# Optimization experiments

Hardware: AMD Instinct MI355X
Metric: run time of the kernel (lower is better)

The kernel has to match this reference:

```python
import jax, jax.numpy as jnp
import numpy as np

IN_DIM, OUT_DIM, NUM, K = 128, 128, 5, 3
SIZE = IN_DIM * OUT_DIM  # number of spline activations
BATCH = 1024


def extend_grid(grid, k):
    # pykan: pad grid by k uniform steps on each side -> (size, num+1+2k)
    h = (grid[:, -1:] - grid[:, :1]) / (grid.shape[1] - 1)
    for _ in range(k):
        grid = jnp.concatenate([grid[:, :1] - h, grid, grid[:, -1:] + h], axis=1)
    return grid


def b_batch(x, grid, k):
    # Cox-de-Boor recursion, unrolled over fixed order k.
    # x: (size, batch), grid: (size, P) already extended. Returns (size, P-1-k, batch).
    x = x[:, None, :]        # (size, 1, batch)
    g = grid[:, :, None]     # (size, P, 1)
    B = ((x >= g[:, :-1]) & (x < g[:, 1:])).astype(x.dtype)  # order 0
    for p in range(1, k + 1):
        B = (x - g[:, :-(p + 1)]) / (g[:, p:-1] - g[:, :-(p + 1)]) * B[:, :-1] \
          + (g[:, p + 1:] - x) / (g[:, p + 1:] - g[:, 1:-p]) * B[:, 1:]
    return B


def setup_inputs() -> dict:
    key = jax.random.key(0)
    k1, k2 = jax.random.split(key)
    x = jax.random.normal(k1, (BATCH, IN_DIM), dtype=jnp.float32)
    # grid: identical uniform rows, as in torch.einsum('i,j->ij', ones(size), linspace)
    grid = jnp.tile(jnp.linspace(-1.0, 1.0, NUM + 1, dtype=jnp.float32)[None, :], (SIZE, 1))
    # coef: (size, num+k) spline coefficients (stand-in for curve2coef init)
    coef = jax.random.normal(k2, (SIZE, NUM + K), dtype=jnp.float32) * 0.1
    scale_base = jnp.ones((SIZE,), jnp.float32)
    scale_sp = jnp.ones((SIZE,), jnp.float32)
    mask = jnp.ones((SIZE,), jnp.float32)
    return {"x": x, "grid": grid, "coef": coef,
            "scale_base": scale_base, "scale_sp": scale_sp, "mask": mask}


def reference(x, grid, coef, scale_base, scale_sp, mask):
    batch = x.shape[0]
    # fan out x over out_dim: einsum('ij,k->ikj').reshape(batch,size).T -> (size, batch)
    xe = jnp.broadcast_to(x[:, None, :], (batch, OUT_DIM, IN_DIM)).reshape(batch, SIZE).T
    preacts = xe.T.reshape(batch, OUT_DIM, IN_DIM)
    base = jax.nn.silu(xe).T                                   # (batch, size)
    B = b_batch(xe, extend_grid(grid, K), K)                   # (size, num+k, batch)
    spline = jnp.einsum('ij,ijk->ik', coef, B).T               # (batch, size)
    postspline = spline.reshape(batch, OUT_DIM, IN_DIM)
    y = mask[None, :] * (scale_base[None, :] * base + scale_sp[None, :] * spline)
    postacts = y.reshape(batch, OUT_DIM, IN_DIM)
    y_out = postacts.sum(axis=2)                               # (batch, out_dim)
    return y_out, preacts, postacts, postspline
```

## Files before the change

### kernel.cpp

```cpp
#include <hip/hip_runtime.h>


#define IN_DIM  128
#define OUT_DIM 128
#define NUMG    5
#define KORD    3
#define NB      8
#define SIZE    (IN_DIM * OUT_DIM)
#define BATCH   1024

__global__ __launch_bounds__(256) void kan_fused(
    const float* __restrict__ x,
    const float* __restrict__ grid,
    const float* __restrict__ coef,
    const float* __restrict__ scale_base,
    const float* __restrict__ scale_sp,
    const float* __restrict__ mask,
    float* __restrict__ out)
{
    __shared__ float sBT[NB][IN_DIM];
    __shared__ float sSilu[IN_DIM];
    __shared__ float sXv[IN_DIM];

    const int tid  = threadIdx.x;
    const int b    = blockIdx.x >> 1;
    const int half = blockIdx.x & 1;

    if (tid < IN_DIM) {
        const int i = tid;
        const float xv = x[b * IN_DIM + i];

        float gr[NUMG + 1];
        #pragma unroll
        for (int r = 0; r <= NUMG; ++r) gr[r] = grid[i * (NUMG + 1) + r];

        const float h = (gr[NUMG] - gr[0]) * (1.0f / NUMG);
        float t[NUMG + 1 + 2 * KORD];
        t[2] = gr[0] - h; t[1] = t[2] - h; t[0] = t[1] - h;
        #pragma unroll
        for (int r = 0; r <= NUMG; ++r) t[KORD + r] = gr[r];
        t[9] = gr[NUMG] + h; t[10] = t[9] + h; t[11] = t[10] + h;

        float B[NUMG + 2 * KORD];
        #pragma unroll
        for (int m = 0; m < NUMG + 2 * KORD; ++m)
            B[m] = (xv >= t[m] && xv < t[m + 1]) ? 1.0f : 0.0f;
        #pragma unroll
        for (int p = 1; p <= KORD; ++p) {
            #pragma unroll
            for (int m = 0; m < NUMG + 2 * KORD - p; ++m) {
                B[m] = (xv - t[m]) / (t[m + p] - t[m]) * B[m]
                     + (t[m + p + 1] - xv) / (t[m + p + 1] - t[m + 1]) * B[m + 1];
            }
        }

        #pragma unroll
        for (int m = 0; m < NB; ++m) sBT[m][i] = B[m];
        sSilu[i] = xv / (1.0f + __expf(-xv));
        sXv[i]   = xv;
    }
    __syncthreads();

    const int lane = tid & 63;
    const int w    = tid >> 6;
    const int il   = lane & 31;
    const int jh   = lane >> 5;
    const int i4   = il << 2;

    float bas[NB][4];
    #pragma unroll
    for (int m = 0; m < NB; ++m) {
        const float4 v = *(const float4*)&sBT[m][i4];
        bas[m][0] = v.x; bas[m][1] = v.y; bas[m][2] = v.z; bas[m][3] = v.w;
    }
    const float4 slv = *(const float4*)&sSilu[i4];
    const float4 pxv = *(const float4*)&sXv[i4];
    const float slA[4] = {slv.x, slv.y, slv.z, slv.w};

    float* out_y   = out;
    float* out_pre = out + BATCH * OUT_DIM;
    float* out_act = out_pre + (size_t)BATCH * SIZE;
    float* out_spl = out_act + (size_t)BATCH * SIZE;

    const int jbase = half * 64 + w * 16 + jh;
    const float4* cp = (const float4*)coef;

    #pragma unroll 2
    for (int jj = 0; jj < 8; ++jj) {
        const int j = jbase + 2 * jj;
        const int s = j * IN_DIM + i4;

        float4 qa[4], qb[4];
        #pragma unroll
        for (int k = 0; k < 4; ++k) {
            qa[k] = cp[2 * (s + k)];
            qb[k] = cp[2 * (s + k) + 1];
        }
        const float4 mkv = *(const float4*)&mask[s];
        const float4 sbv = *(const float4*)&scale_base[s];
        const float4 ssv = *(const float4*)&scale_sp[s];
        const float mkA[4] = {mkv.x, mkv.y, mkv.z, mkv.w};
        const float sbA[4] = {sbv.x, sbv.y, sbv.z, sbv.w};
        const float ssA[4] = {ssv.x, ssv.y, ssv.z, ssv.w};

        float sp[4], y[4];
        #pragma unroll
        for (int k = 0; k < 4; ++k) {
            float r =        qa[k].x * bas[0][k];
            r = fmaf(qa[k].y, bas[1][k], r);
            r = fmaf(qa[k].z, bas[2][k], r);
            r = fmaf(qa[k].w, bas[3][k], r);
            r = fmaf(qb[k].x, bas[4][k], r);
            r = fmaf(qb[k].y, bas[5][k], r);
            r = fmaf(qb[k].z, bas[6][k], r);
            r = fmaf(qb[k].w, bas[7][k], r);
            sp[k] = r;
            y[k]  = mkA[k] * (sbA[k] * slA[k] + ssA[k] * r);
        }

        const size_t e = (size_t)b * SIZE + (size_t)s;
        *(float4*)&out_pre[e] = pxv;
        *(float4*)&out_act[e] = make_float4(y[0], y[1], y[2], y[3]);
        *(float4*)&out_spl[e] = make_float4(sp[0], sp[1], sp[2], sp[3]);

        float acc = (y[0] + y[1]) + (y[2] + y[3]);
        #pragma unroll
        for (int off = 16; off > 0; off >>= 1)
            acc += __shfl_down(acc, off, 32);
        if (il == 0) out_y[b * OUT_DIM + j] = acc;
    }
}

extern "C" void kernel_launch(void* const* d_in, const int* in_sizes, int n_in,
                              void* d_out, int out_size, void* d_ws, size_t ws_size,
                              hipStream_t stream)
{
    hipLaunchKernelGGL(kan_fused, dim3(BATCH * 2), dim3(256), 0, stream,
                       (const float*)d_in[0], (const float*)d_in[1],
                       (const float*)d_in[2], (const float*)d_in[3],
                       (const float*)d_in[4], (const float*)d_in[5],
                       (float*)d_out);
}
```

Before: 255.6 us.

## Coalesce coefficient loads by splitting spline dot product across lane pairs via LDS

```diff
diff --git a/kernel.cpp b/kernel.cpp
--- a/kernel.cpp
+++ b/kernel.cpp
@@ -18,9 +18,10 @@
     const float* __restrict__ mask,
     float* __restrict__ out)
 {
-    __shared__ float sBT[NB][IN_DIM];
+    __shared__ float sB[IN_DIM][NB];
     __shared__ float sSilu[IN_DIM];
     __shared__ float sXv[IN_DIM];
+    __shared__ float sPart[4][2][2][IN_DIM];
 
     const int tid  = threadIdx.x;
     const int b    = blockIdx.x >> 1;
@@ -54,8 +55,8 @@
             }
         }
 
-        #pragma unroll
-        for (int m = 0; m < NB; ++m) sBT[m][i] = B[m];
+        *(float4*)&sB[i][0] = make_float4(B[0], B[1], B[2], B[3]);
+        *(float4*)&sB[i][4] = make_float4(B[4], B[5], B[6], B[7]);
         sSilu[i] = xv / (1.0f + __expf(-xv));
         sXv[i]   = xv;
     }
@@ -63,16 +64,17 @@
 
     const int lane = tid & 63;
     const int w    = tid >> 6;
+    const int a    = lane >> 1;
+    const int mh   = lane & 1;
     const int il   = lane & 31;
     const int jh   = lane >> 5;
     const int i4   = il << 2;
 
-    float bas[NB][4];
+    float4 basq[4];
     #pragma unroll
-    for (int m = 0; m < NB; ++m) {
-        const float4 v = *(const float4*)&sBT[m][i4];
-        bas[m][0] = v.x; bas[m][1] = v.y; bas[m][2] = v.z; bas[m][3] = v.w;
-    }
+    for (int q = 0; q < 4; ++q)
+        basq[q] = *(const float4*)&sB[32 * q + a][4 * mh];
+
     const float4 slv = *(const float4*)&sSilu[i4];
     const float4 pxv = *(const float4*)&sXv[i4];
     const float slA[4] = {slv.x, slv.y, slv.z, slv.w};
@@ -82,52 +84,62 @@
     float* out_act = out_pre + (size_t)BATCH * SIZE;
     float* out_spl = out_act + (size_t)BATCH * SIZE;
 
-    const int jbase = half * 64 + w * 16 + jh;
+    const int jbase = half * 64 + w * 16;
     const float4* cp = (const float4*)coef;
 
     #pragma unroll 2
     for (int jj = 0; jj < 8; ++jj) {
-        const int j = jbase + 2 * jj;
-        const int s = j * IN_DIM + i4;
+        const int j0 = jbase + 2 * jj;
 
-        float4 qa[4], qb[4];
+        float4 cf[2][4];
         #pragma unroll
-        for (int k = 0; k < 4; ++k) {
-            qa[k] = cp[2 * (s + k)];
-            qb[k] = cp[2 * (s + k) + 1];
+        for (int jp = 0; jp < 2; ++jp)
+            #pragma unroll
+            for (int q = 0; q < 4; ++q)
+                cf[jp][q] = cp[(size_t)(j0 + jp) * 256 + 64 * q + lane];
+
+        #pragma unroll
+        for (int jp = 0; jp < 2; ++jp) {
+            #pragma unroll
+            for (int q = 0; q < 4; ++q) {
+                const float4 c = cf[jp][q];
+                const float4 bq = basq[q];
+                float r =        c.x * bq.x;
+                r = fmaf(c.y, bq.y, r);
+                r = fmaf(c.z, bq.z, r);
+                r = fmaf(c.w, bq.w, r);
+                sPart[w][jp][mh][32 * q + a] = r;
+            }
         }
-        const float4 mkv = *(const float4*)&mask[s];
-        const float4 sbv = *(const float4*)&scale_base[s];
-        const float4 ssv = *(const float4*)&scale_sp[s];
+
+        const float4 spE = *(const float4*)&sPart[w][jh][0][i4];
+        const float4 spO = *(const float4*)&sPart[w][jh][1][i4];
+        const float spA[4] = {spE.x + spO.x, spE.y + spO.y,
+                              spE.z + spO.z, spE.w + spO.w};
+
+        const int sS = (j0 + jh) * IN_DIM + i4;
+        const float4 mkv = *(const float4*)&mask[sS];
+        const float4 sbv = *(const float4*)&scale_base[sS];
+        const float4 ssv = *(const float4*)&scale_sp[sS];
         const float mkA[4] = {mkv.x, mkv.y, mkv.z, mkv.w};
         const float sbA[4] = {sbv.x, sbv.y, sbv.z, sbv.w};
         const float ssA[4] = {ssv.x, ssv.y, ssv.z, ssv.w};
 
-        float sp[4], y[4];
+        float y[4];
         #pragma unroll
-        for (int k = 0; k < 4; ++k) {
-            float r =        qa[k].x * bas[0][k];
-            r = fmaf(qa[k].y, bas[1][k], r);
-            r = fmaf(qa[k].z, bas[2][k], r);
-            r = fmaf(qa[k].w, bas[3][k], r);
-            r = fmaf(qb[k].x, bas[4][k], r);
-            r = fmaf(qb[k].y, bas[5][k], r);
-            r = fmaf(qb[k].z, bas[6][k], r);
-            r = fmaf(qb[k].w, bas[7][k], r);
-            sp[k] = r;
-            y[k]  = mkA[k] * (sbA[k] * slA[k] + ssA[k] * r);
-        }
+        for (int k = 0; k < 4; ++k)
+            y[k] = mkA[k] * (sbA[k] * slA[k] + ssA[k] * spA[k]);
 
-        const size_t e = (size_t)b * SIZE + (size_t)s;
+        const size_t e = (size_t)b * SIZE + (size_t)sS;
         *(float4*)&out_pre[e] = pxv;
         *(float4*)&out_act[e] = make_float4(y[0], y[1], y[2], y[3]);
-        *(float4*)&out_spl[e] = make_float4(sp[0], sp[1], sp[2], sp[3]);
+        *(float4*)&out_spl[e] = make_float4(spA[0], spA[1], spA[2], spA[3]);
 
         float acc = (y[0] + y[1]) + (y[2] + y[3]);
         #pragma unroll
         for (int off = 16; off > 0; off >>= 1)
             acc += __shfl_down(acc, off, 32);
-        if (il == 0) out_y[b * OUT_DIM + j] = acc;
+        if (il == 0) out_y[b * OUT_DIM + j0 + jh] = acc;
     }
 }
 
```

New measurement: 220.4 us. -13.8%, faster.
